# Performance work log

Measured on AMD Instinct MI355X. Metric: run time of the kernel, lower is better.

The kernel has to match this reference:

```python
import jax, jax.numpy as jnp
import numpy as np

N = 50000
E = 400000
IN_FEATS = 256
HIDDEN = 64
HEADS = 8
CLASSES = 40
NEG_SLOPE = 0.2  # DGL GATConv default negative_slope


def setup_inputs() -> dict:
    key = jax.random.key(0)
    ks = jax.random.split(key, 12)
    features = jax.random.normal(ks[0], (N, IN_FEATS), dtype=jnp.float32)
    src = jax.random.randint(ks[1], (E,), 0, N, dtype=jnp.int32)
    dst = jax.random.randint(ks[2], (E,), 0, N, dtype=jnp.int32)
    s = 0.05
    # layer 0: in_feats -> HEADS*HIDDEN
    W1 = jax.random.normal(ks[3], (IN_FEATS, HEADS * HIDDEN), dtype=jnp.float32) * s
    al1 = jax.random.normal(ks[4], (HEADS, HIDDEN), dtype=jnp.float32) * s
    ar1 = jax.random.normal(ks[5], (HEADS, HIDDEN), dtype=jnp.float32) * s
    # layer 1: HEADS*HIDDEN -> HEADS*HIDDEN
    W2 = jax.random.normal(ks[6], (HEADS * HIDDEN, HEADS * HIDDEN), dtype=jnp.float32) * s
    al2 = jax.random.normal(ks[7], (HEADS, HIDDEN), dtype=jnp.float32) * s
    ar2 = jax.random.normal(ks[8], (HEADS, HIDDEN), dtype=jnp.float32) * s
    # layer 2: HEADS*HIDDEN -> 1*CLASSES
    W3 = jax.random.normal(ks[9], (HEADS * HIDDEN, CLASSES), dtype=jnp.float32) * s
    al3 = jax.random.normal(ks[10], (1, CLASSES), dtype=jnp.float32) * s
    ar3 = jax.random.normal(ks[11], (1, CLASSES), dtype=jnp.float32) * s
    return {"features": features, "src": src, "dst": dst,
            "W1": W1, "al1": al1, "ar1": ar1,
            "W2": W2, "al2": al2, "ar2": ar2,
            "W3": W3, "al3": al3, "ar3": ar3}


def gat_conv(h, W, al, ar, src, dst):
    """DGL GATConv (no bias, no residual, no activation, no dropout)."""
    H, D = al.shape
    feat = (h @ W).reshape(N, H, D)                      # [N,H,D]
    el = jnp.sum(feat * al[None], axis=-1)               # [N,H]
    er = jnp.sum(feat * ar[None], axis=-1)               # [N,H]
    e = jax.nn.leaky_relu(el[src] + er[dst], NEG_SLOPE)  # [E,H]
    # edge softmax over incoming edges of each dst node
    m = jax.ops.segment_max(e, dst, num_segments=N)      # [N,H]
    ex = jnp.exp(e - m[dst])                             # [E,H]
    denom = jax.ops.segment_sum(ex, dst, num_segments=N) # [N,H]
    alpha = ex / denom[dst]                              # [E,H]
    msg = alpha[:, :, None] * feat[src]                  # [E,H,D]
    out = jax.ops.segment_sum(msg, dst, num_segments=N)  # [N,H,D]
    return out.reshape(N, H * D)


def reference(features, src, dst, W1, al1, ar1, W2, al2, ar2, W3, al3, ar3):
    h = gat_conv(features, W1, al1, ar1, src, dst)  # [N, HEADS*HIDDEN]
    h = gat_conv(h, W2, al2, ar2, src, dst)         # [N, HEADS*HIDDEN]
    h = gat_conv(h, W3, al3, ar3, src, dst)         # [N, CLASSES]
    return h
```

## Files before the change

kernel.cpp:

```cpp
#include <hip/hip_runtime.h>
#include <hip/hip_bf16.h>

#define NN 50000
#define NE 400000
#define MPAD 50048
#define SLOTS 48

typedef __bf16 bf16x8_t __attribute__((ext_vector_type(8)));
typedef __bf16 bf16x4_t __attribute__((ext_vector_type(4)));
typedef float f32x4_t __attribute__((ext_vector_type(4)));

__device__ __forceinline__ float bhi(unsigned int u) {
    union { unsigned int i; float f; } v; v.i = u & 0xffff0000u; return v.f;
}
__device__ __forceinline__ float blo(unsigned int u) {
    union { unsigned int i; float f; } v; v.i = u << 16; return v.f;
}

__global__ __launch_bounds__(256) void prep_kernel(
    const float* __restrict__ W1, __hip_bfloat16* __restrict__ W1t,
    const float* __restrict__ W2, __hip_bfloat16* __restrict__ W2t,
    const float* __restrict__ W3, __hip_bfloat16* __restrict__ W3t,
    const float* __restrict__ al1, const float* __restrict__ ar1,
    const float* __restrict__ al2, const float* __restrict__ ar2,
    __hip_bfloat16* __restrict__ walr1, __hip_bfloat16* __restrict__ walr2) {
    int stride = gridDim.x * blockDim.x;
    for (int i = blockIdx.x * blockDim.x + threadIdx.x; i < 512 * 512; i += stride) {
        if (i < 512 * 256) {
            int n = i >> 8, k = i & 255;
            W1t[i] = __float2bfloat16(W1[k * 512 + n]);
        }
        {
            int n = i >> 9, k = i & 511;
            W2t[i] = __float2bfloat16(W2[k * 512 + n]);
        }
        if (i < 48 * 512) {
            int n = i >> 9, k = i & 511;
            W3t[i] = __float2bfloat16((n < 40) ? W3[k * 40 + n] : 0.f);
        }
        if (i < 16 * 256) {
            int j = i >> 8, k = i & 255;
            const float* v = (j < 8) ? (al1 + j * 64) : (ar1 + (j - 8) * 64);
            float s = 0.f;
            for (int d = 0; d < 64; ++d) s += W1[(size_t)k * 512 + (j & 7) * 64 + d] * v[d];
            walr1[(k >> 5) * 512 + j * 32 + (k & 31)] = __float2bfloat16(s);
        }
        if (i < 16 * 512) {
            int j = i >> 9, k = i & 511;
            const float* v = (j < 8) ? (al2 + j * 64) : (ar2 + (j - 8) * 64);
            float s = 0.f;
            for (int d = 0; d < 64; ++d) s += W2[(size_t)k * 512 + (j & 7) * 64 + d] * v[d];
            walr2[(k >> 5) * 512 + j * 32 + (k & 31)] = __float2bfloat16(s);
        }
    }
}

__global__ void build_kernel(const int* __restrict__ src, const int* __restrict__ dst,
                             int* __restrict__ deg, int* __restrict__ slot) {
    int e = blockIdx.x * blockDim.x + threadIdx.x;
    if (e < NE) {
        int d = dst[e];
        int p = atomicAdd(&deg[d], 1);
        if (p < SLOTS) slot[(size_t)d * SLOTS + p] = src[e];
    }
}

__device__ __forceinline__ void gld_lds16(const void* g, void* l) {
    __builtin_amdgcn_global_load_lds(
        (const __attribute__((address_space(1))) unsigned int*)g,
        (__attribute__((address_space(3))) unsigned int*)l, 16, 0, 0);
}

__global__ __launch_bounds__(256, 2) void gemm1_all(const float* __restrict__ A,
                                                    const __hip_bfloat16* __restrict__ Wt,
                                                    const __hip_bfloat16* __restrict__ walr,
                                                    __hip_bfloat16* __restrict__ C,
                                                    float* __restrict__ el,
                                                    float* __restrict__ er) {
    const int K = 256;
    const int NT = 8;
    __shared__ __align__(16) char smem[2 * 36864];
    const int w = threadIdx.x >> 6;
    const int lane = threadIdx.x & 63;
    const int quad = lane >> 4, l15 = lane & 15;
    const int row0 = blockIdx.x * 64;
    const int srow = lane >> 2;
    const int csrc = ((lane & 3) ^ ((lane >> 3) & 3)) * 8;
    const int rswz = l15 * 64 + ((quad ^ ((l15 >> 1) & 3)) << 4);

    int arow = row0 + w * 16 + srow;
    int rc = (arow < NN) ? arow : (NN - 1);
    const float* gA = A + (size_t)rc * K + csrc;
    const __hip_bfloat16* gBb = Wt + (size_t)(w * 128 + srow) * K + csrc;

    f32x4_t acc[4][8] = {};
    f32x4_t acce[4] = {};
    float4 curA0, curA1, nxtA0, nxtA1;

    curA0 = *reinterpret_cast<const float4*>(gA);
    curA1 = *reinterpret_cast<const float4*>(gA + 4);
    {
        char* buf = smem;
#pragma unroll
        for (int o = 0; o < 8; ++o)
            gld_lds16(gBb + (size_t)o * 16 * K, buf + 4096 + (w * 8 + o) * 1024);
    }

#pragma unroll
    for (int t = 0; t < NT; ++t) {
        char* buf = smem + (t & 1) * 36864;
        bf16x8_t b5;
        if (w == 0) {
            b5 = *reinterpret_cast<const bf16x8_t*>(walr + t * 512 + l15 * 32 + quad * 8);
            asm volatile("" ::: "memory");
        }
        if (t + 1 < NT) {
            char* nb = smem + ((t + 1) & 1) * 36864;
            const int k1 = (t + 1) * 32;
            nxtA0 = *reinterpret_cast<const float4*>(gA + k1);
            nxtA1 = *reinterpret_cast<const float4*>(gA + k1 + 4);
#pragma unroll
            for (int o = 0; o < 8; ++o)
                gld_lds16(gBb + (size_t)o * 16 * K + k1, nb + 4096 + (w * 8 + o) * 1024);
            asm volatile("s_waitcnt vmcnt(10)" ::: "memory");
        } else {
            asm volatile("s_waitcnt vmcnt(0)" ::: "memory");
        }
        {
            bf16x8_t h;
            h[0] = (__bf16)curA0.x; h[1] = (__bf16)curA0.y;
            h[2] = (__bf16)curA0.z; h[3] = (__bf16)curA0.w;
            h[4] = (__bf16)curA1.x; h[5] = (__bf16)curA1.y;
            h[6] = (__bf16)curA1.z; h[7] = (__bf16)curA1.w;
            *reinterpret_cast<bf16x8_t*>(buf + w * 1024 + lane * 16) = h;
        }
        curA0 = nxtA0; curA1 = nxtA1;
        asm volatile("s_waitcnt lgkmcnt(0)" ::: "memory");
        __builtin_amdgcn_s_barrier();
        asm volatile("" ::: "memory");
        bf16x8_t a[4], b[8];
#pragma unroll
        for (int mi = 0; mi < 4; mi++)
            a[mi] = *reinterpret_cast<const bf16x8_t*>(buf + mi * 1024 + rswz);
#pragma unroll
        for (int ni = 0; ni < 8; ni++)
            b[ni] = *reinterpret_cast<const bf16x8_t*>(buf + 4096 + (w * 8 + ni) * 1024 + rswz);
#pragma unroll
        for (int mi = 0; mi < 4; mi++)
#pragma unroll
            for (int ni = 0; ni < 8; ni++)
                acc[mi][ni] = __builtin_amdgcn_mfma_f32_16x16x32_bf16(a[mi], b[ni], acc[mi][ni], 0, 0, 0);
        if (w == 0) {
#pragma unroll
            for (int mi = 0; mi < 4; mi++)
                acce[mi] = __builtin_amdgcn_mfma_f32_16x16x32_bf16(a[mi], b5, acce[mi], 0, 0, 0);
        }
        asm volatile("" ::: "memory");
        __builtin_amdgcn_s_barrier();
        asm volatile("" ::: "memory");
    }

#pragma unroll
    for (int mi = 0; mi < 4; mi++) {
#pragma unroll
        for (int ni = 0; ni < 8; ni++) {
#pragma unroll
            for (int r = 0; r < 4; r++) {
                int row = row0 + mi * 16 + quad * 4 + r;
                if (row < NN)
                    C[(size_t)row * 512 + w * 128 + ni * 16 + l15] =
                        __float2bfloat16(acc[mi][ni][r]);
            }
        }
    }
    if (w == 0) {
#pragma unroll
        for (int mi = 0; mi < 4; mi++) {
#pragma unroll
            for (int r = 0; r < 4; r++) {
                int row = row0 + mi * 16 + quad * 4 + r;
                if (row < NN) {
                    float v = acce[mi][r];
                    if (l15 < 8) el[row * 8 + l15] = v;
                    else er[row * 8 + l15 - 8] = v;
                }
            }
        }
    }
}

template <int K>
__global__ __launch_bounds__(256, 2) void gemm_all(const __hip_bfloat16* __restrict__ A,
                                                   const __hip_bfloat16* __restrict__ Wt,
                                                   const __hip_bfloat16* __restrict__ walr,
                                                   __hip_bfloat16* __restrict__ C,
                                                   float* __restrict__ el,
                                                   float* __restrict__ er) {
    const int NT = K / 32;
    __shared__ __align__(16) char smem[2 * 36864];
    const int w = threadIdx.x >> 6;
    const int lane = threadIdx.x & 63;
    const int quad = lane >> 4, l15 = lane & 15;
    const int row0 = blockIdx.x * 64;
    const int srow = lane >> 2;
    const int csrc = ((lane & 3) ^ ((lane >> 3) & 3)) * 8;
    const int rswz = l15 * 64 + ((quad ^ ((l15 >> 1) & 3)) << 4);

    const __hip_bfloat16* gA = A + (size_t)(row0 + w * 16 + srow) * K + csrc;
    const __hip_bfloat16* gBb = Wt + (size_t)(w * 128 + srow) * K + csrc;

    f32x4_t acc[4][8] = {};
    f32x4_t acce[4] = {};

    {
        char* buf = smem;
        gld_lds16(gA, buf + w * 1024);
#pragma unroll
        for (int o = 0; o < 8; ++o)
            gld_lds16(gBb + (size_t)o * 16 * K, buf + 4096 + (w * 8 + o) * 1024);
    }

#pragma unroll
    for (int t = 0; t < NT; ++t) {
        char* buf = smem + (t & 1) * 36864;
        bf16x8_t b5;
        if (w == 0) {
            b5 = *reinterpret_cast<const bf16x8_t*>(walr + t * 512 + l15 * 32 + quad * 8);
            asm volatile("" ::: "memory");
        }
        if (t + 1 < NT) {
            char* nb = smem + ((t + 1) & 1) * 36864;
            const int k1 = (t + 1) * 32;
            gld_lds16(gA + k1, nb + w * 1024);
#pragma unroll
            for (int o = 0; o < 8; ++o)
                gld_lds16(gBb + (size_t)o * 16 * K + k1, nb + 4096 + (w * 8 + o) * 1024);
            asm volatile("s_waitcnt vmcnt(9)" ::: "memory");
        } else {
            asm volatile("s_waitcnt vmcnt(0)" ::: "memory");
        }
        __builtin_amdgcn_s_barrier();
        asm volatile("" ::: "memory");
        bf16x8_t a[4], b[8];
#pragma unroll
        for (int mi = 0; mi < 4; mi++)
            a[mi] = *reinterpret_cast<const bf16x8_t*>(buf + mi * 1024 + rswz);
#pragma unroll
        for (int ni = 0; ni < 8; ni++)
            b[ni] = *reinterpret_cast<const bf16x8_t*>(buf + 4096 + (w * 8 + ni) * 1024 + rswz);
#pragma unroll
        for (int mi = 0; mi < 4; mi++)
#pragma unroll
            for (int ni = 0; ni < 8; ni++)
                acc[mi][ni] = __builtin_amdgcn_mfma_f32_16x16x32_bf16(a[mi], b[ni], acc[mi][ni], 0, 0, 0);
        if (w == 0) {
#pragma unroll
            for (int mi = 0; mi < 4; mi++)
                acce[mi] = __builtin_amdgcn_mfma_f32_16x16x32_bf16(a[mi], b5, acce[mi], 0, 0, 0);
        }
        asm volatile("" ::: "memory");
        __builtin_amdgcn_s_barrier();
        asm volatile("" ::: "memory");
    }

#pragma unroll
    for (int mi = 0; mi < 4; mi++) {
#pragma unroll
        for (int ni = 0; ni < 8; ni++) {
#pragma unroll
            for (int r = 0; r < 4; r++) {
                int row = row0 + mi * 16 + quad * 4 + r;
                if (row < NN)
                    C[(size_t)row * 512 + w * 128 + ni * 16 + l15] =
                        __float2bfloat16(acc[mi][ni][r]);
            }
        }
    }
    if (w == 0) {
#pragma unroll
        for (int mi = 0; mi < 4; mi++) {
#pragma unroll
            for (int r = 0; r < 4; r++) {
                int row = row0 + mi * 16 + quad * 4 + r;
                if (row < NN) {
                    float v = acce[mi][r];
                    if (l15 < 8) el[row * 8 + l15] = v;
                    else er[row * 8 + l15 - 8] = v;
                }
            }
        }
    }
}

#define W3_LDSROW 520
__global__ __launch_bounds__(256) void gemm3_mfma(const __hip_bfloat16* __restrict__ A,
                                                  const __hip_bfloat16* __restrict__ W3t,
                                                  const float* __restrict__ al,
                                                  const float* __restrict__ ar,
                                                  __hip_bfloat16* __restrict__ C,
                                                  float* __restrict__ el,
                                                  float* __restrict__ er) {
    __shared__ __align__(16) __hip_bfloat16 wlds[48 * W3_LDSROW];
    for (int c = threadIdx.x; c < 48 * 64; c += 256) {
        int n = c >> 6, koff = (c & 63) * 8;
        *reinterpret_cast<uint4*>(&wlds[n * W3_LDSROW + koff]) =
            *reinterpret_cast<const uint4*>(W3t + n * 512 + koff);
    }
    __syncthreads();
    const int w = threadIdx.x >> 6;
    const int lane = threadIdx.x & 63;
    const int quad = lane >> 4, l15 = lane & 15;
    const int row0 = blockIdx.x * 64 + w * 16;

    float alv[3], arv[3];
#pragma unroll
    for (int c = 0; c < 3; c++) {
        int col = c * 16 + l15;
        alv[c] = (col < 40) ? al[col] : 0.f;
        arv[c] = (col < 40) ? ar[col] : 0.f;
    }

    f32x4_t acc[3] = {};
    const __hip_bfloat16* arow = A + (size_t)(row0 + l15) * 512;
#pragma unroll 4
    for (int k0 = 0; k0 < 512; k0 += 32) {
        bf16x8_t a = *reinterpret_cast<const bf16x8_t*>(arow + k0 + quad * 8);
#pragma unroll
        for (int c = 0; c < 3; c++) {
            bf16x8_t b = *reinterpret_cast<const bf16x8_t*>(
                &wlds[(c * 16 + l15) * W3_LDSROW + k0 + quad * 8]);
            acc[c] = __builtin_amdgcn_mfma_f32_16x16x32_bf16(a, b, acc[c], 0, 0, 0);
        }
    }
#pragma unroll
    for (int r = 0; r < 4; r++) {
        int row = row0 + quad * 4 + r;
        bool rok = row < NN;
        float pl = 0.f, pr = 0.f;
#pragma unroll
        for (int c = 0; c < 3; c++) {
            float v = acc[c][r];
            if (rok) C[(size_t)row * 64 + c * 16 + l15] = __float2bfloat16(v);
            pl += v * alv[c];
            pr += v * arv[c];
        }
        if (rok) C[(size_t)row * 64 + 48 + l15] = __float2bfloat16(0.f);
        pl += __shfl_xor(pl, 1, 64); pr += __shfl_xor(pr, 1, 64);
        pl += __shfl_xor(pl, 2, 64); pr += __shfl_xor(pr, 2, 64);
        pl += __shfl_xor(pl, 4, 64); pr += __shfl_xor(pr, 4, 64);
        pl += __shfl_xor(pl, 8, 64); pr += __shfl_xor(pr, 8, 64);
        if (l15 == 0 && rok) { el[row] = pl; er[row] = pr; }
    }
}

__device__ __forceinline__ void fma8(float* acc, float pj, const uint4& q) {
    acc[0] += pj * blo(q.x); acc[1] += pj * bhi(q.x);
    acc[2] += pj * blo(q.y); acc[3] += pj * bhi(q.y);
    acc[4] += pj * blo(q.z); acc[5] += pj * bhi(q.z);
    acc[6] += pj * blo(q.w); acc[7] += pj * bhi(q.w);
}

__global__ __launch_bounds__(256) void agg8_kernel(const __hip_bfloat16* __restrict__ feat,
                                                   const float* __restrict__ el,
                                                   const float* __restrict__ er,
                                                   const int* __restrict__ deg,
                                                   const int* __restrict__ slot,
                                                   __hip_bfloat16* __restrict__ out) {
    int n = (blockIdx.x * blockDim.x + threadIdx.x) >> 6;
    int lane = threadIdx.x & 63;
    if (n >= NN) return;
    const int es = lane >> 3;
    const int h8 = lane & 7;
    const int hd = lane >> 3;
    int dn = min(deg[n], SLOTS);
    __hip_bfloat16* orow = out + (size_t)n * 512 + lane * 8;
    if (dn == 0) {
        bf16x8_t z = {};
        __builtin_nontemporal_store(z, reinterpret_cast<bf16x8_t*>(orow));
        return;
    }
    float er_n = er[n * 8 + h8];
    const int* sl = slot + (size_t)n * SLOTS;
    int slv = sl[lane < dn ? lane : dn - 1];
    const int dm = dn - 1;
    const int nr = (dn + 7) >> 3;

    float pr[6];
    float lsum = 0.f;
#pragma unroll
    for (int r = 0; r < 6; ++r) {
        pr[r] = 0.f;
        if (r < nr) {
            int e = r * 8 + es;
            bool valid = e < dn;
            int s = __shfl(slv, valid ? e : 0, 64);
            float t = el[s * 8 + h8] + er_n;
            float x = (t >= 0.f) ? t : 0.2f * t;
            pr[r] = valid ? __expf(x) : 0.f;
        }
        lsum += pr[r];
    }
    lsum += __shfl_xor(lsum, 8, 64);
    lsum += __shfl_xor(lsum, 16, 64);
    lsum += __shfl_xor(lsum, 32, 64);
    float lh = __shfl(lsum, hd, 64);
    float inv = (lh > 0.f) ? 1.f / lh : 0.f;

    float acc[8] = {};
#pragma unroll
    for (int r = 0; r < 6; ++r) {
        if (r < nr) {
            const int b8 = r * 8;
            int s0 = __builtin_amdgcn_readlane(slv, min(b8 + 0, dm));
            int s1 = __builtin_amdgcn_readlane(slv, min(b8 + 1, dm));
            int s2 = __builtin_amdgcn_readlane(slv, min(b8 + 2, dm));
            int s3 = __builtin_amdgcn_readlane(slv, min(b8 + 3, dm));
            int s4 = __builtin_amdgcn_readlane(slv, min(b8 + 4, dm));
            int s5 = __builtin_amdgcn_readlane(slv, min(b8 + 5, dm));
            int s6 = __builtin_amdgcn_readlane(slv, min(b8 + 6, dm));
            int s7 = __builtin_amdgcn_readlane(slv, min(b8 + 7, dm));
            uint4 q0 = *reinterpret_cast<const uint4*>(feat + (size_t)s0 * 512 + lane * 8);
            uint4 q1 = *reinterpret_cast<const uint4*>(feat + (size_t)s1 * 512 + lane * 8);
            uint4 q2 = *reinterpret_cast<const uint4*>(feat + (size_t)s2 * 512 + lane * 8);
            uint4 q3 = *reinterpret_cast<const uint4*>(feat + (size_t)s3 * 512 + lane * 8);
            uint4 q4 = *reinterpret_cast<const uint4*>(feat + (size_t)s4 * 512 + lane * 8);
            uint4 q5 = *reinterpret_cast<const uint4*>(feat + (size_t)s5 * 512 + lane * 8);
            uint4 q6 = *reinterpret_cast<const uint4*>(feat + (size_t)s6 * 512 + lane * 8);
            uint4 q7 = *reinterpret_cast<const uint4*>(feat + (size_t)s7 * 512 + lane * 8);
            float p0 = __shfl(pr[r], 0 * 8 + hd, 64); fma8(acc, p0, q0);
            float p1 = __shfl(pr[r], 1 * 8 + hd, 64); fma8(acc, p1, q1);
            float p2 = __shfl(pr[r], 2 * 8 + hd, 64); fma8(acc, p2, q2);
            float p3 = __shfl(pr[r], 3 * 8 + hd, 64); fma8(acc, p3, q3);
            float p4 = __shfl(pr[r], 4 * 8 + hd, 64); fma8(acc, p4, q4);
            float p5 = __shfl(pr[r], 5 * 8 + hd, 64); fma8(acc, p5, q5);
            float p6 = __shfl(pr[r], 6 * 8 + hd, 64); fma8(acc, p6, q6);
            float p7 = __shfl(pr[r], 7 * 8 + hd, 64); fma8(acc, p7, q7);
        }
    }
    bf16x8_t o8;
#pragma unroll
    for (int d = 0; d < 8; ++d) o8[d] = (__bf16)(acc[d] * inv);
    __builtin_nontemporal_store(o8, reinterpret_cast<bf16x8_t*>(orow));
}

__global__ __launch_bounds__(256) void agg3_kernel(const __hip_bfloat16* __restrict__ feat,
                                                   const float* __restrict__ el,
                                                   const float* __restrict__ er,
                                                   const int* __restrict__ deg,
                                                   const int* __restrict__ slot,
                                                   float* __restrict__ out) {
    int n = (blockIdx.x * blockDim.x + threadIdx.x) >> 6;
    int lane = threadIdx.x & 63;
    if (n >= NN) return;
    const int es = lane >> 3;
    const int dc = lane & 7;
    int dn = min(deg[n], SLOTS);
    float er_n = er[n];
    const int* sl = slot + (size_t)n * SLOTS;

    float lsum = 0.f;
    float acc[8] = {};
    for (int base = 0; base < dn; base += 16) {
        int e0 = base + es, e1 = base + 8 + es;
        bool v0 = e0 < dn, v1 = e1 < dn;
        int s0 = v0 ? sl[e0] : 0;
        int s1 = v1 ? sl[e1] : 0;
        float t0 = el[s0] + er_n;
        float t1 = el[s1] + er_n;
        float x0 = (t0 >= 0.f) ? t0 : 0.2f * t0;
        float x1 = (t1 >= 0.f) ? t1 : 0.2f * t1;
        float p0 = v0 ? __expf(x0) : 0.f;
        float p1 = v1 ? __expf(x1) : 0.f;
        lsum += p0 + p1;
        uint4 q0 = *reinterpret_cast<const uint4*>(feat + (size_t)s0 * 64 + dc * 8);
        uint4 q1 = *reinterpret_cast<const uint4*>(feat + (size_t)s1 * 64 + dc * 8);
        acc[0] += p0 * blo(q0.x) + p1 * blo(q1.x);
        acc[1] += p0 * bhi(q0.x) + p1 * bhi(q1.x);
        acc[2] += p0 * blo(q0.y) + p1 * blo(q1.y);
        acc[3] += p0 * bhi(q0.y) + p1 * bhi(q1.y);
        acc[4] += p0 * blo(q0.z) + p1 * blo(q1.z);
        acc[5] += p0 * bhi(q0.z) + p1 * bhi(q1.z);
        acc[6] += p0 * blo(q0.w) + p1 * blo(q1.w);
        acc[7] += p0 * bhi(q0.w) + p1 * bhi(q1.w);
    }
    lsum += __shfl_xor(lsum, 8, 64);
    lsum += __shfl_xor(lsum, 16, 64);
    lsum += __shfl_xor(lsum, 32, 64);
#pragma unroll
    for (int d = 0; d < 8; ++d) {
        acc[d] += __shfl_xor(acc[d], 8, 64);
        acc[d] += __shfl_xor(acc[d], 16, 64);
        acc[d] += __shfl_xor(acc[d], 32, 64);
    }
    float inv = (lsum > 0.f) ? 1.f / lsum : 0.f;
    if (es == 0 && dc < 5) {
        float4 o0 = make_float4(acc[0] * inv, acc[1] * inv, acc[2] * inv, acc[3] * inv);
        float4 o1 = make_float4(acc[4] * inv, acc[5] * inv, acc[6] * inv, acc[7] * inv);
        *reinterpret_cast<float4*>(out + (size_t)n * 40 + dc * 8) = o0;
        *reinterpret_cast<float4*>(out + (size_t)n * 40 + dc * 8 + 4) = o1;
    }
}

extern "C" void kernel_launch(void* const* d_in, const int* in_sizes, int n_in,
                              void* d_out, int out_size, void* d_ws, size_t ws_size,
                              hipStream_t stream) {
    const float* features = (const float*)d_in[0];
    const int* src = (const int*)d_in[1];
    const int* dst = (const int*)d_in[2];
    const float* W1 = (const float*)d_in[3];
    const float* al1 = (const float*)d_in[4];
    const float* ar1 = (const float*)d_in[5];
    const float* W2 = (const float*)d_in[6];
    const float* al2 = (const float*)d_in[7];
    const float* ar2 = (const float*)d_in[8];
    const float* W3 = (const float*)d_in[9];
    const float* al3 = (const float*)d_in[10];
    const float* ar3 = (const float*)d_in[11];

    char* ws = (char*)d_ws;
    size_t o = 0;
    auto carve = [&](size_t bytes) -> void* {
        o = (o + 255) & ~(size_t)255;
        void* p = ws + o;
        o += bytes;
        return p;
    };
    __hip_bfloat16* Fbf = (__hip_bfloat16*)carve((size_t)MPAD * 512 * 2);
    __hip_bfloat16* Gbf = (__hip_bfloat16*)carve((size_t)MPAD * 512 * 2);
    __hip_bfloat16* W1t = (__hip_bfloat16*)carve((size_t)512 * 256 * 2);
    __hip_bfloat16* W2t = (__hip_bfloat16*)carve((size_t)512 * 512 * 2);
    __hip_bfloat16* W3t = (__hip_bfloat16*)carve((size_t)48 * 512 * 2);
    __hip_bfloat16* walr1 = (__hip_bfloat16*)carve((size_t)16 * 256 * 2);
    __hip_bfloat16* walr2 = (__hip_bfloat16*)carve((size_t)16 * 512 * 2);
    float* el = (float*)carve((size_t)NN * 8 * 4);
    float* er = (float*)carve((size_t)NN * 8 * 4);
    float* el3 = (float*)carve((size_t)NN * 4);
    float* er3 = (float*)carve((size_t)NN * 4);
    int* deg = (int*)carve((size_t)NN * 4);
    int* slot = (int*)carve((size_t)NN * SLOTS * 4);

    hipMemsetAsync(deg, 0, (size_t)NN * 4, stream);
    build_kernel<<<(NE + 255) / 256, 256, 0, stream>>>(src, dst, deg, slot);
    prep_kernel<<<512, 256, 0, stream>>>(W1, W1t, W2, W2t, W3, W3t,
                                         al1, ar1, al2, ar2, walr1, walr2);

    const int gmm = MPAD / 64;
    gemm1_all<<<gmm, 256, 0, stream>>>(features, W1t, walr1, Fbf, el, er);
    agg8_kernel<<<(NN + 3) / 4, 256, 0, stream>>>(Fbf, el, er, deg, slot, Gbf);
    gemm_all<512><<<gmm, 256, 0, stream>>>(Gbf, W2t, walr2, Fbf, el, er);
    agg8_kernel<<<(NN + 3) / 4, 256, 0, stream>>>(Fbf, el, er, deg, slot, Gbf);
    gemm3_mfma<<<MPAD / 64, 256, 0, stream>>>(Gbf, W3t, al3, ar3, Fbf, el3, er3);
    agg3_kernel<<<(NN + 3) / 4, 256, 0, stream>>>(Fbf, el3, er3, deg, slot, (float*)d_out);
}
```

Measured before the change: 404.7 us.

## Replace LDS double-buffered GEMMs with register-direct MFMA loads and 2D grid

The layer-1 and layer-2 GEMMs drop LDS staging, double buffering and barriers, and instead load A and B fragments straight from global memory into registers for MFMA. The grid gains a second dimension that splits the 512 output columns in two, so each block computes a 64x256 tile with 64 columns per wave, halving per-thread accumulators and raising occupancy. The aim is to remove barrier and LDS overhead. In exchange, A tiles are reloaded from global memory by every wave and by both column blocks, which adds load traffic that relies on the cache and loses the explicit load/compute overlap.

Measured after the change: 511.1 us. 1.26x slower.

```diff
diff --git a/kernel.cpp b/kernel.cpp
--- a/kernel.cpp
+++ b/kernel.cpp
@@ -65,115 +65,76 @@
     }
 }
 
-__device__ __forceinline__ void gld_lds16(const void* g, void* l) {
-    __builtin_amdgcn_global_load_lds(
-        (const __attribute__((address_space(1))) unsigned int*)g,
-        (__attribute__((address_space(3))) unsigned int*)l, 16, 0, 0);
-}
-
-__global__ __launch_bounds__(256, 2) void gemm1_all(const float* __restrict__ A,
-                                                    const __hip_bfloat16* __restrict__ Wt,
-                                                    const __hip_bfloat16* __restrict__ walr,
-                                                    __hip_bfloat16* __restrict__ C,
-                                                    float* __restrict__ el,
-                                                    float* __restrict__ er) {
+__global__ __launch_bounds__(256) void gemm1_reg(const float* __restrict__ A,
+                                                 const __hip_bfloat16* __restrict__ Wt,
+                                                 const __hip_bfloat16* __restrict__ walr,
+                                                 __hip_bfloat16* __restrict__ C,
+                                                 float* __restrict__ el,
+                                                 float* __restrict__ er) {
     const int K = 256;
-    const int NT = 8;
-    __shared__ __align__(16) char smem[2 * 36864];
     const int w = threadIdx.x >> 6;
     const int lane = threadIdx.x & 63;
     const int quad = lane >> 4, l15 = lane & 15;
     const int row0 = blockIdx.x * 64;
-    const int srow = lane >> 2;
-    const int csrc = ((lane & 3) ^ ((lane >> 3) & 3)) * 8;
-    const int rswz = l15 * 64 + ((quad ^ ((l15 >> 1) & 3)) << 4);
-
-    int arow = row0 + w * 16 + srow;
-    int rc = (arow < NN) ? arow : (NN - 1);
-    const float* gA = A + (size_t)rc * K + csrc;
-    const __hip_bfloat16* gBb = Wt + (size_t)(w * 128 + srow) * K + csrc;
-
-    f32x4_t acc[4][8] = {};
+    const int colw = blockIdx.y * 256 + w * 64;
+    const bool my_e = (blockIdx.y == 0) && (w == 0);
+
+    const float* baseA[4];
+    const __hip_bfloat16* baseB[4];
+#pragma unroll
+    for (int mi = 0; mi < 4; mi++) {
+        int r = row0 + mi * 16 + l15;
+        if (r >= NN) r = NN - 1;
+        baseA[mi] = A + (size_t)r * K + quad * 8;
+    }
+#pragma unroll
+    for (int ni = 0; ni < 4; ni++)
+        baseB[ni] = Wt + (size_t)(colw + ni * 16 + l15) * K + quad * 8;
+
+    f32x4_t acc[4][4] = {};
     f32x4_t acce[4] = {};
-    float4 curA0, curA1, nxtA0, nxtA1;
-
-    curA0 = *reinterpret_cast<const float4*>(gA);
-    curA1 = *reinterpret_cast<const float4*>(gA + 4);
-    {
-        char* buf = smem;
-#pragma unroll
-        for (int o = 0; o < 8; ++o)
-            gld_lds16(gBb + (size_t)o * 16 * K, buf + 4096 + (w * 8 + o) * 1024);
-    }
-
-#pragma unroll
-    for (int t = 0; t < NT; ++t) {
-        char* buf = smem + (t & 1) * 36864;
-        bf16x8_t b5;
-        if (w == 0) {
-            b5 = *reinterpret_cast<const bf16x8_t*>(walr + t * 512 + l15 * 32 + quad * 8);
-            asm volatile("" ::: "memory");
-        }
-        if (t + 1 < NT) {
-            char* nb = smem + ((t + 1) & 1) * 36864;
-            const int k1 = (t + 1) * 32;
-            nxtA0 = *reinterpret_cast<const float4*>(gA + k1);
-            nxtA1 = *reinterpret_cast<const float4*>(gA + k1 + 4);
-#pragma unroll
-            for (int o = 0; o < 8; ++o)
-                gld_lds16(gBb + (size_t)o * 16 * K + k1, nb + 4096 + (w * 8 + o) * 1024);
-            asm volatile("s_waitcnt vmcnt(10)" ::: "memory");
-        } else {
-            asm volatile("s_waitcnt vmcnt(0)" ::: "memory");
-        }
-        {
-            bf16x8_t h;
-            h[0] = (__bf16)curA0.x; h[1] = (__bf16)curA0.y;
-            h[2] = (__bf16)curA0.z; h[3] = (__bf16)curA0.w;
-            h[4] = (__bf16)curA1.x; h[5] = (__bf16)curA1.y;
-            h[6] = (__bf16)curA1.z; h[7] = (__bf16)curA1.w;
-            *reinterpret_cast<bf16x8_t*>(buf + w * 1024 + lane * 16) = h;
-        }
-        curA0 = nxtA0; curA1 = nxtA1;
-        asm volatile("s_waitcnt lgkmcnt(0)" ::: "memory");
-        __builtin_amdgcn_s_barrier();
-        asm volatile("" ::: "memory");
-        bf16x8_t a[4], b[8];
+#pragma unroll
+    for (int t = 0; t < K / 32; ++t) {
+        const int k0 = t * 32;
+        bf16x8_t a[4], b[4];
+#pragma unroll
+        for (int mi = 0; mi < 4; mi++) {
+            float4 f0 = *reinterpret_cast<const float4*>(baseA[mi] + k0);
+            float4 f1 = *reinterpret_cast<const float4*>(baseA[mi] + k0 + 4);
+            a[mi][0] = (__bf16)f0.x; a[mi][1] = (__bf16)f0.y;
+            a[mi][2] = (__bf16)f0.z; a[mi][3] = (__bf16)f0.w;
+            a[mi][4] = (__bf16)f1.x; a[mi][5] = (__bf16)f1.y;
+            a[mi][6] = (__bf16)f1.z; a[mi][7] = (__bf16)f1.w;
+        }
+#pragma unroll
+        for (int ni = 0; ni < 4; ni++)
+            b[ni] = *reinterpret_cast<const bf16x8_t*>(baseB[ni] + k0);
 #pragma unroll
         for (int mi = 0; mi < 4; mi++)
-            a[mi] = *reinterpret_cast<const bf16x8_t*>(buf + mi * 1024 + rswz);
-#pragma unroll
-        for (int ni = 0; ni < 8; ni++)
-            b[ni] = *reinterpret_cast<const bf16x8_t*>(buf + 4096 + (w * 8 + ni) * 1024 + rswz);
-#pragma unroll
-        for (int mi = 0; mi < 4; mi++)
-#pragma unroll
-            for (int ni = 0; ni < 8; ni++)
+#pragma unroll
+            for (int ni = 0; ni < 4; ni++)
                 acc[mi][ni] = __builtin_amdgcn_mfma_f32_16x16x32_bf16(a[mi], b[ni], acc[mi][ni], 0, 0, 0);
-        if (w == 0) {
+        if (my_e) {
+            bf16x8_t b5 = *reinterpret_cast<const bf16x8_t*>(walr + t * 512 + l15 * 32 + quad * 8);
 #pragma unroll
             for (int mi = 0; mi < 4; mi++)
                 acce[mi] = __builtin_amdgcn_mfma_f32_16x16x32_bf16(a[mi], b5, acce[mi], 0, 0, 0);
         }
-        asm volatile("" ::: "memory");
-        __builtin_amdgcn_s_barrier();
-        asm volatile("" ::: "memory");
-    }
-
+    }
 #pragma unroll
     for (int mi = 0; mi < 4; mi++) {
 #pragma unroll
-        for (int ni = 0; ni < 8; ni++) {
+        for (int ni = 0; ni < 4; ni++) {
 #pragma unroll
             for (int r = 0; r < 4; r++) {
                 int row = row0 + mi * 16 + quad * 4 + r;
                 if (row < NN)
-                    C[(size_t)row * 512 + w * 128 + ni * 16 + l15] =
+                    C[(size_t)row * 512 + colw + ni * 16 + l15] =
                         __float2bfloat16(acc[mi][ni][r]);
             }
         }
     }
-    if (w == 0) {
+    if (my_e) {
 #pragma unroll
         for (int mi = 0; mi < 4; mi++) {
 #pragma unroll
@@ -190,93 +151,69 @@
 }
 
 template <int K>
-__global__ __launch_bounds__(256, 2) void gemm_all(const __hip_bfloat16* __restrict__ A,
-                                                   const __hip_bfloat16* __restrict__ Wt,
-                                                   const __hip_bfloat16* __restrict__ walr,
-                                                   __hip_bfloat16* __restrict__ C,
-                                                   float* __restrict__ el,
-                                                   float* __restrict__ er) {
-    const int NT = K / 32;
-    __shared__ __align__(16) char smem[2 * 36864];
+__global__ __launch_bounds__(256) void gemm_reg(const __hip_bfloat16* __restrict__ A,
+                                                const __hip_bfloat16* __restrict__ Wt,
+                                                const __hip_bfloat16* __restrict__ walr,
+                                                __hip_bfloat16* __restrict__ C,
+                                                float* __restrict__ el,
+                                                float* __restrict__ er) {
     const int w = threadIdx.x >> 6;
     const int lane = threadIdx.x & 63;
     const int quad = lane >> 4, l15 = lane & 15;
     const int row0 = blockIdx.x * 64;
-    const int srow = lane >> 2;
-    const int csrc = ((lane & 3) ^ ((lane >> 3) & 3)) * 8;
-    const int rswz = l15 * 64 + ((quad ^ ((l15 >> 1) & 3)) << 4);
-
-    const __hip_bfloat16* gA = A + (size_t)(row0 + w * 16 + srow) * K + csrc;
-    const __hip_bfloat16* gBb = Wt + (size_t)(w * 128 + srow) * K + csrc;
-
-    f32x4_t acc[4][8] = {};
+    const int colw = blockIdx.y * 256 + w * 64;
+    const bool my_e = (blockIdx.y == 0) && (w == 0);
+
+    const __hip_bfloat16* baseA[4];
+    const __hip_bfloat16* baseB[4];
+#pragma unroll
+    for (int mi = 0; mi < 4; mi++) {
+        int r = row0 + mi * 16 + l15;
+        if (r >= NN) r = NN - 1;
+        baseA[mi] = A + (size_t)r * K + quad * 8;
+    }
+#pragma unroll
+    for (int ni = 0; ni < 4; ni++)
+        baseB[ni] = Wt + (size_t)(colw + ni * 16 + l15) * K + quad * 8;
+
+    f32x4_t acc[4][4] = {};
     f32x4_t acce[4] = {};
-
-    {
-        char* buf = smem;
-        gld_lds16(gA, buf + w * 1024);
-#pragma unroll
-        for (int o = 0; o < 8; ++o)
-            gld_lds16(gBb + (size_t)o * 16 * K, buf + 4096 + (w * 8 + o) * 1024);
-    }
-
-#pragma unroll
-    for (int t = 0; t < NT; ++t) {
-        char* buf = smem + (t & 1) * 36864;
-        bf16x8_t b5;
-        if (w == 0) {
-            b5 = *reinterpret_cast<const bf16x8_t*>(walr + t * 512 + l15 * 32 + quad * 8);
-            asm volatile("" ::: "memory");
-        }
-        if (t + 1 < NT) {
-            char* nb = smem + ((t + 1) & 1) * 36864;
-            const int k1 = (t + 1) * 32;
-            gld_lds16(gA + k1, nb + w * 1024);
-#pragma unroll
-            for (int o = 0; o < 8; ++o)
-                gld_lds16(gBb + (size_t)o * 16 * K + k1, nb + 4096 + (w * 8 + o) * 1024);
-            asm volatile("s_waitcnt vmcnt(9)" ::: "memory");
-        } else {
-            asm volatile("s_waitcnt vmcnt(0)" ::: "memory");
-        }
-        __builtin_amdgcn_s_barrier();
-        asm volatile("" ::: "memory");
-        bf16x8_t a[4], b[8];
+#pragma unroll
+    for (int t = 0; t < K / 32; ++t) {
+        const int k0 = t * 32;
+        bf16x8_t a[4], b[4];
 #pragma unroll
         for (int mi = 0; mi < 4; mi++)
-            a[mi] = *reinterpret_cast<const bf16x8_t*>(buf + mi * 1024 + rswz);
-#pragma unroll
-        for (int ni = 0; ni < 8; ni++)
-            b[ni] = *reinterpret_cast<const bf16x8_t*>(buf + 4096 + (w * 8 + ni) * 1024 + rswz);
+            a[mi] = *reinterpret_cast<const bf16x8_t*>(baseA[mi] + k0);
+#pragma unroll
+        for (int ni = 0; ni < 4; ni++)
+            b[ni] = *reinterpret_cast<const bf16x8_t*>(baseB[ni] + k0);
 #pragma unroll
         for (int mi = 0; mi < 4; mi++)
 #pragma unroll
-            for (int ni = 0; ni < 8; ni++)
+            for (int ni = 0; ni < 4; ni++)
                 acc[mi][ni] = __builtin_amdgcn_mfma_f32_16x16x32_bf16(a[mi], b[ni], acc[mi][ni], 0, 0, 0);
-        if (w == 0) {
+        if (my_e) {
+            bf16x8_t b5 = *reinterpret_cast<const bf16x8_t*>(walr + t * 512 + l15 * 32 + quad * 8);
 #pragma unroll
             for (int mi = 0; mi < 4; mi++)
                 acce[mi] = __builtin_amdgcn_mfma_f32_16x16x32_bf16(a[mi], b5, acce[mi], 0, 0, 0);
         }
-        asm volatile("" ::: "memory");
-        __builtin_amdgcn_s_barrier();
-        asm volatile("" ::: "memory");
-    }
-
+    }
 #pragma unroll
     for (int mi = 0; mi < 4; mi++) {
 #pragma unroll
-        for (int ni = 0; ni < 8; ni++) {
+        for (int ni = 0; ni < 4; ni++) {
 #pragma unroll
             for (int r = 0; r < 4; r++) {
                 int row = row0 + mi * 16 + quad * 4 + r;
                 if (row < NN)
-                    C[(size_t)row * 512 + w * 128 + ni * 16 + l15] =
+                    C[(size_t)row * 512 + colw + ni * 16 + l15] =
                         __float2bfloat16(acc[mi][ni][r]);
             }
         }
     }
-    if (w == 0) {
+    if (my_e) {
 #pragma unroll
         for (int mi = 0; mi < 4; mi++) {
 #pragma unroll
@@ -545,9 +482,9 @@
                                          al1, ar1, al2, ar2, walr1, walr2);
 
     const int gmm = MPAD / 64;
-    gemm1_all<<<gmm, 256, 0, stream>>>(features, W1t, walr1, Fbf, el, er);
+    gemm1_reg<<<dim3(gmm, 2), 256, 0, stream>>>(features, W1t, walr1, Fbf, el, er);
     agg8_kernel<<<(NN + 3) / 4, 256, 0, stream>>>(Fbf, el, er, deg, slot, Gbf);
-    gemm_all<512><<<gmm, 256, 0, stream>>>(Gbf, W2t, walr2, Fbf, el, er);
+    gemm_reg<512><<<dim3(gmm, 2), 256, 0, stream>>>(Gbf, W2t, walr2, Fbf, el, er);
     agg8_kernel<<<(NN + 3) / 4, 256, 0, stream>>>(Fbf, el, er, deg, slot, Gbf);
     gemm3_mfma<<<MPAD / 64, 256, 0, stream>>>(Gbf, W3t, al3, ar3, Fbf, el3, er3);
     agg3_kernel<<<(NN + 3) / 4, 256, 0, stream>>>(Fbf, el3, er3, deg, slot, (float*)d_out);
```
